# Optimization experiments

Measured on AMD Instinct MI355X. Metric: run time of the kernel, lower is better.

Reference implementation:

```python
import jax, jax.numpy as jnp
import numpy as np

NUM_USERS = 400000  # matches fill_max of indexes in input_specs
K = 10              # top_k from init_kwargs
NEG_INF = -1000000000.0


def setup_inputs() -> dict:
    key = jax.random.key(0)
    k1, k2, k3 = jax.random.split(key, 3)
    N = 8000000
    predictions = jax.random.normal(k1, (N,), dtype=jnp.float32)
    targets = jax.random.uniform(k2, (N,), dtype=jnp.float32)
    indexes = jax.random.randint(k3, (N,), 0, NUM_USERS, dtype=jnp.int64)
    return {"predictions": predictions, "targets": targets, "indexes": indexes}


def reference(predictions, targets, indexes):
    # Faithful to the torch source, which does `counts_per_user[u] = 1` (not +=1):
    # column 0 holds each user's FIRST occurrence, column 1 holds the LAST
    # occurrence (subsequent scatters to pos 1 overwrite), everything else is
    # padding (-1e9 preds / 0 targets). Padding columns beyond k provably don't
    # affect topk/dcg/idcg, so we use a static width of K.
    n = predictions.shape[0]
    pos = jnp.arange(n, dtype=jnp.int32)
    seg = indexes.astype(jnp.int32)
    first = jax.ops.segment_min(pos, seg, num_segments=NUM_USERS)
    last = jax.ops.segment_max(pos, seg, num_segments=NUM_USERS)
    counts = jax.ops.segment_sum(jnp.ones_like(pos), seg, num_segments=NUM_USERS)
    has2 = counts >= 2  # pos 1 is only ever written on a second occurrence

    p0 = predictions[first]
    t0 = targets[first]
    p1 = jnp.where(has2, predictions[last], NEG_INF)
    t1 = jnp.where(has2, targets[last], 0.0)

    pred_padded = jnp.full((NUM_USERS, K), NEG_INF, dtype=predictions.dtype)
    pred_padded = pred_padded.at[:, 0].set(p0).at[:, 1].set(p1)
    target_padded = jnp.zeros((NUM_USERS, K), dtype=targets.dtype)
    target_padded = target_padded.at[:, 0].set(t0).at[:, 1].set(t1)

    _, topk_idx = jax.lax.top_k(pred_padded, K)
    topk_targets = jnp.take_along_axis(target_padded, topk_idx, axis=1)
    discounts = jnp.log2(jnp.arange(2, K + 2, dtype=jnp.float32))
    dcg = (topk_targets / discounts).sum(axis=1)
    ideal = -jnp.sort(-target_padded, axis=1)  # descending sort
    idcg = (ideal[:, :K] / discounts).sum(axis=1)
    return (dcg / idcg).mean()
```

## Files before the change

### kernel.cpp

```cpp
#include <hip/hip_runtime.h>
#include <climits>

static constexpr int NUSERS = 400000;
static constexpr float NEG_INF_F = -1000000000.0f;
static constexpr float INV_LOG2_3 = 0.6309297535714575f;

static constexpr int USLICE = 1563;
static constexpr int S = 256;
static constexpr int CHUNK = 4096;
static constexpr int CPG = 255;
static constexpr int GSPAN = CHUNK * CPG;
static constexpr int G = 8;
static constexpr int CAP = 4608;


__global__ void k_init_part(int* __restrict__ cursor, float* __restrict__ acc) {
    int t = blockIdx.x * blockDim.x + threadIdx.x;
    if (t < G * S) cursor[t] = 0;
    if (t == G * S) acc[0] = 0.0f;
}

__global__ __launch_bounds__(256, 8) void k_scatter(const int* __restrict__ idx, int n,
                                                    unsigned* __restrict__ records,
                                                    int* __restrict__ cursor) {
    __shared__ int cnt[S];
    __shared__ int base_l[S + 1];
    __shared__ int base_g[S];
    __shared__ unsigned stage[CHUNK];

    const int t = threadIdx.x;
    const int g = blockIdx.x / CPG;
    const int cbase = blockIdx.x * CHUNK - g * GSPAN;
    const int q0 = blockIdx.x * (CHUNK / 4);
    const int nq = n >> 2;
    const int4* idx4 = reinterpret_cast<const int4*>(idx);

    int4 v[4];
    int rnk[16];
#pragma unroll
    for (int k = 0; k < 4; ++k) {
        int q = q0 + k * 256 + t;
        v[k] = (q < nq) ? idx4[q] : make_int4(-1, -1, -1, -1);
    }

    if (t < S) cnt[t] = 0;
    __syncthreads();

#pragma unroll
    for (int k = 0; k < 4; ++k) {
        int us[4] = {v[k].x, v[k].y, v[k].z, v[k].w};
#pragma unroll
        for (int e = 0; e < 4; ++e)
            rnk[k * 4 + e] = (us[e] >= 0) ? atomicAdd(&cnt[us[e] / USLICE], 1) : 0;
    }
    __syncthreads();

    if (t < 64) {
        int v0 = cnt[t];
        int v1 = cnt[64 + t];
        int v2 = cnt[128 + t];
        int v3 = cnt[192 + t];
        int a = v0, b = v1, c = v2, d = v3;
#pragma unroll
        for (int dd = 1; dd < 64; dd <<= 1) { int y = __shfl_up(a, dd, 64); if (t >= dd) a += y; }
        int ta = __shfl(a, 63, 64);
#pragma unroll
        for (int dd = 1; dd < 64; dd <<= 1) { int y = __shfl_up(b, dd, 64); if (t >= dd) b += y; }
        int tb = __shfl(b, 63, 64);
#pragma unroll
        for (int dd = 1; dd < 64; dd <<= 1) { int y = __shfl_up(c, dd, 64); if (t >= dd) c += y; }
        int tc = __shfl(c, 63, 64);
#pragma unroll
        for (int dd = 1; dd < 64; dd <<= 1) { int y = __shfl_up(d, dd, 64); if (t >= dd) d += y; }
        int td = __shfl(d, 63, 64);
        b += ta; c += ta + tb; d += ta + tb + tc;
        base_l[t] = a - v0;
        base_l[64 + t] = b - v1;
        base_l[128 + t] = c - v2;
        base_l[192 + t] = d - v3;
        if (t == 0) base_l[S] = ta + tb + tc + td;
    }
    if (t < S) base_g[t] = atomicAdd(&cursor[g * S + t], cnt[t]);
    __syncthreads();

#pragma unroll
    for (int k = 0; k < 4; ++k) {
        int us[4] = {v[k].x, v[k].y, v[k].z, v[k].w};
#pragma unroll
        for (int e = 0; e < 4; ++e) {
            int u = us[e];
            if (u >= 0) {
                int s = u / USLICE;
                int loc = u - s * USLICE;
                int pos = base_l[s] + rnk[k * 4 + e];
                unsigned pic = (unsigned)((k * 256 + t) * 4 + e);
                stage[pos] = ((unsigned)s << 23) | ((unsigned)loc << 12) | pic;
            }
        }
    }
    __syncthreads();

    int total = base_l[S];
    for (int r = t; r < total; r += 256) {
        unsigned tmp = stage[r];
        int s = tmp >> 23;
        unsigned loc = (tmp >> 12) & 0x7FFu;
        unsigned iloc = (unsigned)cbase + (tmp & 0xFFFu);
        int pos = base_g[s] + (r - base_l[s]);
        if (pos < CAP)
            records[(size_t)(g * S + s) * CAP + pos] = (loc << 20) | iloc;
    }
}

__global__ __launch_bounds__(1024, 4) void k_reduce_ndcg(
        const unsigned* __restrict__ records, const int* __restrict__ cursor,
        const float* __restrict__ pred, const float* __restrict__ tgt,
        int n, float* __restrict__ acc) {
    __shared__ int tabf[USLICE];
    __shared__ int tabl[USLICE];
    const int s = blockIdx.x;
    const int t = threadIdx.x;

    for (int u = t; u < USLICE; u += 1024) { tabf[u] = INT_MAX; tabl[u] = -1; }
    __syncthreads();

    for (int g = 0; g < G; ++g) {
        int cnt = min(cursor[g * S + s], CAP);
        const uint4* base4 = reinterpret_cast<const uint4*>(records + (size_t)(g * S + s) * CAP);
        const int gb = g * GSPAN;
        for (int p4 = t; p4 * 4 < cnt; p4 += 1024) {
            uint4 vv = base4[p4];
            int p = p4 * 4;
            unsigned rr[4] = {vv.x, vv.y, vv.z, vv.w};
#pragma unroll
            for (int e = 0; e < 4; ++e) {
                if (p + e < cnt) {
                    int loc = rr[e] >> 20;
                    int i = (int)(rr[e] & 0xFFFFFu) + gb;
                    atomicMin(&tabf[loc], i);
                    atomicMax(&tabl[loc], i);
                }
            }
        }
    }
    __syncthreads();

    float v = 0.0f;
    for (int uu = t; uu < USLICE; uu += 1024) {
        int u = s * USLICE + uu;
        if (u < NUSERS) {
            int f = tabf[uu];
            int l = tabl[uu];
            f = min(f, n - 1);
            float p0 = pred[f];
            float t0 = tgt[f];
            bool has2 = l > f;
            float p1 = has2 ? pred[l] : NEG_INF_F;
            float t1 = has2 ? tgt[l] : 0.0f;
            float dcg  = (p0 >= p1) ? fmaf(t1, INV_LOG2_3, t0) : fmaf(t0, INV_LOG2_3, t1);
            float idcg = fmaf(fminf(t0, t1), INV_LOG2_3, fmaxf(t0, t1));
            v += dcg / idcg;
        }
    }
    for (int off = 32; off > 0; off >>= 1) v += __shfl_down(v, off, 64);
    __shared__ float wsum[16];
    int lane = t & 63, wid = t >> 6;
    if (lane == 0) wsum[wid] = v;
    __syncthreads();
    if (t == 0) {
        float ss = 0.0f;
#pragma unroll
        for (int w = 0; w < 16; ++w) ss += wsum[w];
        atomicAdd(acc, ss);
    }
}

__global__ void k_final(const float* __restrict__ acc, float* __restrict__ out) {
    out[0] = acc[0] * (1.0f / (float)NUSERS);
}


__global__ void k_init_fb(int* __restrict__ first, int* __restrict__ last,
                          float* __restrict__ acc) {
    int i = blockIdx.x * blockDim.x + threadIdx.x;
    if (i < NUSERS) { first[i] = INT_MAX; last[i] = -1; }
    if (i == 0) acc[0] = 0.0f;
}

__global__ void k_minmax_fb(const int* __restrict__ idx, int* __restrict__ first,
                            int* __restrict__ last, int n) {
    int base = (blockIdx.x * blockDim.x + threadIdx.x) * 4;
    if (base + 3 < n) {
        int4 u4 = *reinterpret_cast<const int4*>(idx + base);
        int us[4] = {u4.x, u4.y, u4.z, u4.w};
#pragma unroll
        for (int j = 0; j < 4; ++j) {
            int u = us[j], i = base + j;
            if (i < first[u]) atomicMin(&first[u], i);
            if (i > last[u])  atomicMax(&last[u], i);
        }
    } else {
        for (int i = base; i < n; ++i) {
            int u = idx[i];
            if (i < first[u]) atomicMin(&first[u], i);
            if (i > last[u])  atomicMax(&last[u], i);
        }
    }
}

__global__ void k_ndcg_fb(const float* __restrict__ pred, const float* __restrict__ tgt,
                          const int* __restrict__ first, const int* __restrict__ last,
                          int n, float* __restrict__ acc) {
    int u = blockIdx.x * blockDim.x + threadIdx.x;
    float v = 0.0f;
    if (u < NUSERS) {
        int f = min(first[u], n - 1);
        int l = last[u];
        float p0 = pred[f], t0 = tgt[f];
        bool has2 = l > f;
        float p1 = has2 ? pred[l] : NEG_INF_F;
        float t1 = has2 ? tgt[l] : 0.0f;
        float dcg  = (p0 >= p1) ? fmaf(t1, INV_LOG2_3, t0) : fmaf(t0, INV_LOG2_3, t1);
        float idcg = fmaf(fminf(t0, t1), INV_LOG2_3, fmaxf(t0, t1));
        v = dcg / idcg;
    }
    for (int off = 32; off > 0; off >>= 1) v += __shfl_down(v, off, 64);
    __shared__ float wsum[4];
    int lane = threadIdx.x & 63, wid = threadIdx.x >> 6;
    if (lane == 0) wsum[wid] = v;
    __syncthreads();
    if (threadIdx.x == 0) atomicAdd(acc, wsum[0] + wsum[1] + wsum[2] + wsum[3]);
}


extern "C" void kernel_launch(void* const* d_in, const int* in_sizes, int n_in,
                              void* d_out, int out_size, void* d_ws, size_t ws_size,
                              hipStream_t stream) {
    const float* pred = (const float*)d_in[0];
    const float* tgt  = (const float*)d_in[1];
    const int*   idx  = (const int*)d_in[2];
    const int n = in_sizes[0];
    float* out = (float*)d_out;

    const size_t recs_bytes = (size_t)G * S * CAP * sizeof(unsigned);
    const size_t need = recs_bytes + 16384;

    if (ws_size >= need && n <= G * GSPAN && (n & 3) == 0) {
        unsigned* records = (unsigned*)d_ws;
        char* tail = (char*)d_ws + recs_bytes;
        int* cursor = (int*)tail;
        float* acc = (float*)(tail + 8192);

        k_init_part<<<(G * S + 256) / 256, 256, 0, stream>>>(cursor, acc);

        int nblocks = (n + CHUNK - 1) / CHUNK;
        k_scatter<<<nblocks, 256, 0, stream>>>(idx, n, records, cursor);

        k_reduce_ndcg<<<S, 1024, 0, stream>>>(records, cursor, pred, tgt, n, acc);

        k_final<<<1, 1, 0, stream>>>(acc, out);
    } else {
        int* first = (int*)d_ws;
        int* last  = first + NUSERS;
        float* acc = (float*)(last + NUSERS);

        k_init_fb<<<(NUSERS + 255) / 256, 256, 0, stream>>>(first, last, acc);
        int nq4 = (n + 3) / 4;
        k_minmax_fb<<<(nq4 + 255) / 256, 256, 0, stream>>>(idx, first, last, n);
        k_ndcg_fb<<<(NUSERS + 255) / 256, 256, 0, stream>>>(pred, tgt, first, last, n, acc);
        k_final<<<1, 1, 0, stream>>>(acc, out);
    }
}
```

Baseline: 151.1 us.

## Replace partitioned scatter with global atomic min/max plus value-capture pass

Drops the two-pass slice partition (LDS bucket scatter to records, then per-slice LDS min/max reduce) and replaces it with direct global atomicMin/atomicMax on an interleaved int2 first/last table. Chunks are visited in a hashed order so concurrent blocks touch scattered users, which reduces atomic contention. A second streaming pass reads idx, pred and tgt coalesced and writes the (pred, tgt) pairs for the first and last occurrence into a per-user table, removing the random gathers. The final NDCG kernel does the normalisation itself through a last-block counter, which removes k_final. In exchange it adds a full extra read of the 8M indices plus pred and tgt, and relies on global atomics that may contend.

New measurement: 509.6 us. 237% more time.

```diff
diff --git a/kernel.cpp b/kernel.cpp
--- a/kernel.cpp
+++ b/kernel.cpp
@@ -5,231 +5,128 @@
 static constexpr float NEG_INF_F = -1000000000.0f;
 static constexpr float INV_LOG2_3 = 0.6309297535714575f;
 
-static constexpr int USLICE = 1563;
-static constexpr int S = 256;
-static constexpr int CHUNK = 4096;
-static constexpr int CPG = 255;
-static constexpr int GSPAN = CHUNK * CPG;
-static constexpr int G = 8;
-static constexpr int CAP = 4608;
+static constexpr int NB1 = 2048;
+static constexpr int CE_LOG2 = 11;
+static constexpr int CE = 1 << CE_LOG2;
 
-
-__global__ void k_init_part(int* __restrict__ cursor, float* __restrict__ acc) {
-    int t = blockIdx.x * blockDim.x + threadIdx.x;
-    if (t < G * S) cursor[t] = 0;
-    if (t == G * S) acc[0] = 0.0f;
+__global__ void k_init(int2* __restrict__ tab, float2* __restrict__ vals,
+                       const float* __restrict__ pred, const float* __restrict__ tgt,
+                       int n, int* __restrict__ ctrl, float* __restrict__ acc) {
+    int i = blockIdx.x * blockDim.x + threadIdx.x;
+    float pl = pred[n - 1], tl = tgt[n - 1];
+    if (i < NUSERS) {
+        tab[i] = make_int2(INT_MAX, -1);
+        vals[2 * i]     = make_float2(pl, tl);
+        vals[2 * i + 1] = make_float2(NEG_INF_F, 0.0f);
+    }
+    if (i == 0) { ctrl[0] = 0; acc[0] = 0.0f; }
 }
 
-__global__ __launch_bounds__(256, 8) void k_scatter(const int* __restrict__ idx, int n,
-                                                    unsigned* __restrict__ records,
-                                                    int* __restrict__ cursor) {
-    __shared__ int cnt[S];
-    __shared__ int base_l[S + 1];
-    __shared__ int base_g[S];
-    __shared__ unsigned stage[CHUNK];
-
-    const int t = threadIdx.x;
-    const int g = blockIdx.x / CPG;
-    const int cbase = blockIdx.x * CHUNK - g * GSPAN;
-    const int q0 = blockIdx.x * (CHUNK / 4);
+__global__ __launch_bounds__(256, 8) void k_minmax(const int* __restrict__ idx, int n,
+                                                   int2* __restrict__ tab,
+                                                   unsigned pmask) {
     const int nq = n >> 2;
     const int4* idx4 = reinterpret_cast<const int4*>(idx);
+    const int t = threadIdx.x;
 
-    int4 v[4];
-    int rnk[16];
+    for (unsigned k = blockIdx.x; k <= pmask; k += NB1) {
+        unsigned chunk = (k * 0x9E3779B1u) & pmask;
+        int q0 = (int)(chunk << (CE_LOG2 - 2));
+        if (q0 >= nq) continue;
+
+        int4 v[2];
 #pragma unroll
-    for (int k = 0; k < 4; ++k) {
-        int q = q0 + k * 256 + t;
-        v[k] = (q < nq) ? idx4[q] : make_int4(-1, -1, -1, -1);
+        for (int r = 0; r < 2; ++r) {
+            int q = q0 + r * 256 + t;
+            v[r] = (q < nq) ? idx4[q] : make_int4(-1, -1, -1, -1);
+        }
+        int us[8] = {v[0].x, v[0].y, v[0].z, v[0].w,
+                     v[1].x, v[1].y, v[1].z, v[1].w};
+        int2 cur[8];
+#pragma unroll
+        for (int j = 0; j < 8; ++j)
+            cur[j] = (us[j] >= 0) ? tab[us[j]] : make_int2(INT_MIN, INT_MAX);
+#pragma unroll
+        for (int j = 0; j < 8; ++j) {
+            int r = j >> 2, e = j & 3;
+            int i = (q0 + r * 256 + t) * 4 + e;
+            if (i < cur[j].x) atomicMin(&tab[us[j]].x, i);
+            if (us[j] >= 0 && i > cur[j].y) atomicMax(&tab[us[j]].y, i);
+        }
     }
+    if (blockIdx.x == 0 && t == 0) {
+        for (int i = nq * 4; i < n; ++i) {
+            int u = idx[i];
+            atomicMin(&tab[u].x, i);
+            atomicMax(&tab[u].y, i);
+        }
+    }
+}
 
-    if (t < S) cnt[t] = 0;
-    __syncthreads();
-
+__global__ __launch_bounds__(256, 8) void k_detect(const int* __restrict__ idx,
+        const float* __restrict__ pred, const float* __restrict__ tgt, int n,
+        const int2* __restrict__ tab, float2* __restrict__ vals) {
+    const int nq = n >> 2;
+    const int4* idx4 = reinterpret_cast<const int4*>(idx);
+    const float4* pred4 = reinterpret_cast<const float4*>(pred);
+    const float4* tgt4 = reinterpret_cast<const float4*>(tgt);
+    const int t = threadIdx.x;
 #pragma unroll
-    for (int k = 0; k < 4; ++k) {
-        int us[4] = {v[k].x, v[k].y, v[k].z, v[k].w};
+    for (int r = 0; r < 2; ++r) {
+        int q = blockIdx.x * 512 + r * 256 + t;
+        if (q < nq) {
+            int4 u4 = idx4[q];
+            float4 p4 = pred4[q];
+            float4 g4 = tgt4[q];
+            int us[4] = {u4.x, u4.y, u4.z, u4.w};
+            float ps[4] = {p4.x, p4.y, p4.z, p4.w};
+            float gs[4] = {g4.x, g4.y, g4.z, g4.w};
+            int ib = q * 4;
 #pragma unroll
-        for (int e = 0; e < 4; ++e)
-            rnk[k * 4 + e] = (us[e] >= 0) ? atomicAdd(&cnt[us[e] / USLICE], 1) : 0;
-    }
-    __syncthreads();
-
-    if (t < 64) {
-        int v0 = cnt[t];
-        int v1 = cnt[64 + t];
-        int v2 = cnt[128 + t];
-        int v3 = cnt[192 + t];
-        int a = v0, b = v1, c = v2, d = v3;
-#pragma unroll
-        for (int dd = 1; dd < 64; dd <<= 1) { int y = __shfl_up(a, dd, 64); if (t >= dd) a += y; }
-        int ta = __shfl(a, 63, 64);
-#pragma unroll
-        for (int dd = 1; dd < 64; dd <<= 1) { int y = __shfl_up(b, dd, 64); if (t >= dd) b += y; }
-        int tb = __shfl(b, 63, 64);
-#pragma unroll
-        for (int dd = 1; dd < 64; dd <<= 1) { int y = __shfl_up(c, dd, 64); if (t >= dd) c += y; }
-        int tc = __shfl(c, 63, 64);
-#pragma unroll
-        for (int dd = 1; dd < 64; dd <<= 1) { int y = __shfl_up(d, dd, 64); if (t >= dd) d += y; }
-        int td = __shfl(d, 63, 64);
-        b += ta; c += ta + tb; d += ta + tb + tc;
-        base_l[t] = a - v0;
-        base_l[64 + t] = b - v1;
-        base_l[128 + t] = c - v2;
-        base_l[192 + t] = d - v3;
-        if (t == 0) base_l[S] = ta + tb + tc + td;
-    }
-    if (t < S) base_g[t] = atomicAdd(&cursor[g * S + t], cnt[t]);
-    __syncthreads();
-
-#pragma unroll
-    for (int k = 0; k < 4; ++k) {
-        int us[4] = {v[k].x, v[k].y, v[k].z, v[k].w};
-#pragma unroll
-        for (int e = 0; e < 4; ++e) {
-            int u = us[e];
-            if (u >= 0) {
-                int s = u / USLICE;
-                int loc = u - s * USLICE;
-                int pos = base_l[s] + rnk[k * 4 + e];
-                unsigned pic = (unsigned)((k * 256 + t) * 4 + e);
-                stage[pos] = ((unsigned)s << 23) | ((unsigned)loc << 12) | pic;
+            for (int e = 0; e < 4; ++e) {
+                int u = us[e];
+                int2 fl = tab[u];
+                int i = ib + e;
+                if (i == fl.x)      vals[2 * u]     = make_float2(ps[e], gs[e]);
+                else if (i == fl.y) vals[2 * u + 1] = make_float2(ps[e], gs[e]);
             }
         }
     }
-    __syncthreads();
-
-    int total = base_l[S];
-    for (int r = t; r < total; r += 256) {
-        unsigned tmp = stage[r];
-        int s = tmp >> 23;
-        unsigned loc = (tmp >> 12) & 0x7FFu;
-        unsigned iloc = (unsigned)cbase + (tmp & 0xFFFu);
-        int pos = base_g[s] + (r - base_l[s]);
-        if (pos < CAP)
-            records[(size_t)(g * S + s) * CAP + pos] = (loc << 20) | iloc;
+    if (blockIdx.x == 0 && t == 0) {
+        for (int i = nq * 4; i < n; ++i) {
+            int u = idx[i];
+            int2 fl = tab[u];
+            if (i == fl.x)      vals[2 * u]     = make_float2(pred[i], tgt[i]);
+            else if (i == fl.y) vals[2 * u + 1] = make_float2(pred[i], tgt[i]);
+        }
     }
 }
 
-__global__ __launch_bounds__(1024, 4) void k_reduce_ndcg(
-        const unsigned* __restrict__ records, const int* __restrict__ cursor,
-        const float* __restrict__ pred, const float* __restrict__ tgt,
-        int n, float* __restrict__ acc) {
-    __shared__ int tabf[USLICE];
-    __shared__ int tabl[USLICE];
-    const int s = blockIdx.x;
+__global__ __launch_bounds__(256, 8) void k_ndcg(const float4* __restrict__ vals,
+        float* __restrict__ acc, int* __restrict__ ctrl, float* __restrict__ out,
+        int nblk) {
     const int t = threadIdx.x;
-
-    for (int u = t; u < USLICE; u += 1024) { tabf[u] = INT_MAX; tabl[u] = -1; }
-    __syncthreads();
-
-    for (int g = 0; g < G; ++g) {
-        int cnt = min(cursor[g * S + s], CAP);
-        const uint4* base4 = reinterpret_cast<const uint4*>(records + (size_t)(g * S + s) * CAP);
-        const int gb = g * GSPAN;
-        for (int p4 = t; p4 * 4 < cnt; p4 += 1024) {
-            uint4 vv = base4[p4];
-            int p = p4 * 4;
-            unsigned rr[4] = {vv.x, vv.y, vv.z, vv.w};
-#pragma unroll
-            for (int e = 0; e < 4; ++e) {
-                if (p + e < cnt) {
-                    int loc = rr[e] >> 20;
-                    int i = (int)(rr[e] & 0xFFFFFu) + gb;
-                    atomicMin(&tabf[loc], i);
-                    atomicMax(&tabl[loc], i);
-                }
-            }
-        }
-    }
-    __syncthreads();
-
+    int u = blockIdx.x * 256 + t;
     float v = 0.0f;
-    for (int uu = t; uu < USLICE; uu += 1024) {
-        int u = s * USLICE + uu;
-        if (u < NUSERS) {
-            int f = tabf[uu];
-            int l = tabl[uu];
-            f = min(f, n - 1);
-            float p0 = pred[f];
-            float t0 = tgt[f];
-            bool has2 = l > f;
-            float p1 = has2 ? pred[l] : NEG_INF_F;
-            float t1 = has2 ? tgt[l] : 0.0f;
-            float dcg  = (p0 >= p1) ? fmaf(t1, INV_LOG2_3, t0) : fmaf(t0, INV_LOG2_3, t1);
-            float idcg = fmaf(fminf(t0, t1), INV_LOG2_3, fmaxf(t0, t1));
-            v += dcg / idcg;
-        }
+    if (u < NUSERS) {
+        float4 w = vals[u];
+        float dcg  = (w.x >= w.z) ? fmaf(w.w, INV_LOG2_3, w.y) : fmaf(w.y, INV_LOG2_3, w.w);
+        float idcg = fmaf(fminf(w.y, w.w), INV_LOG2_3, fmaxf(w.y, w.w));
+        v = dcg / idcg;
     }
     for (int off = 32; off > 0; off >>= 1) v += __shfl_down(v, off, 64);
-    __shared__ float wsum[16];
+    __shared__ float wsum[4];
     int lane = t & 63, wid = t >> 6;
     if (lane == 0) wsum[wid] = v;
     __syncthreads();
     if (t == 0) {
-        float ss = 0.0f;
-#pragma unroll
-        for (int w = 0; w < 16; ++w) ss += wsum[w];
-        atomicAdd(acc, ss);
-    }
-}
-
-__global__ void k_final(const float* __restrict__ acc, float* __restrict__ out) {
-    out[0] = acc[0] * (1.0f / (float)NUSERS);
-}
-
-
-__global__ void k_init_fb(int* __restrict__ first, int* __restrict__ last,
-                          float* __restrict__ acc) {
-    int i = blockIdx.x * blockDim.x + threadIdx.x;
-    if (i < NUSERS) { first[i] = INT_MAX; last[i] = -1; }
-    if (i == 0) acc[0] = 0.0f;
-}
-
-__global__ void k_minmax_fb(const int* __restrict__ idx, int* __restrict__ first,
-                            int* __restrict__ last, int n) {
-    int base = (blockIdx.x * blockDim.x + threadIdx.x) * 4;
-    if (base + 3 < n) {
-        int4 u4 = *reinterpret_cast<const int4*>(idx + base);
-        int us[4] = {u4.x, u4.y, u4.z, u4.w};
-#pragma unroll
-        for (int j = 0; j < 4; ++j) {
-            int u = us[j], i = base + j;
-            if (i < first[u]) atomicMin(&first[u], i);
-            if (i > last[u])  atomicMax(&last[u], i);
-        }
-    } else {
-        for (int i = base; i < n; ++i) {
-            int u = idx[i];
-            if (i < first[u]) atomicMin(&first[u], i);
-            if (i > last[u])  atomicMax(&last[u], i);
+        atomicAdd(acc, wsum[0] + wsum[1] + wsum[2] + wsum[3]);
+        int d = __hip_atomic_fetch_add(&ctrl[0], 1, __ATOMIC_ACQ_REL, __HIP_MEMORY_SCOPE_AGENT);
+        if (d == nblk - 1) {
+            float a = __hip_atomic_load(acc, __ATOMIC_RELAXED, __HIP_MEMORY_SCOPE_AGENT);
+            out[0] = a * (1.0f / (float)NUSERS);
         }
     }
-}
-
-__global__ void k_ndcg_fb(const float* __restrict__ pred, const float* __restrict__ tgt,
-                          const int* __restrict__ first, const int* __restrict__ last,
-                          int n, float* __restrict__ acc) {
-    int u = blockIdx.x * blockDim.x + threadIdx.x;
-    float v = 0.0f;
-    if (u < NUSERS) {
-        int f = min(first[u], n - 1);
-        int l = last[u];
-        float p0 = pred[f], t0 = tgt[f];
-        bool has2 = l > f;
-        float p1 = has2 ? pred[l] : NEG_INF_F;
-        float t1 = has2 ? tgt[l] : 0.0f;
-        float dcg  = (p0 >= p1) ? fmaf(t1, INV_LOG2_3, t0) : fmaf(t0, INV_LOG2_3, t1);
-        float idcg = fmaf(fminf(t0, t1), INV_LOG2_3, fmaxf(t0, t1));
-        v = dcg / idcg;
-    }
-    for (int off = 32; off > 0; off >>= 1) v += __shfl_down(v, off, 64);
-    __shared__ float wsum[4];
-    int lane = threadIdx.x & 63, wid = threadIdx.x >> 6;
-    if (lane == 0) wsum[wid] = v;
-    __syncthreads();
-    if (threadIdx.x == 0) atomicAdd(acc, wsum[0] + wsum[1] + wsum[2] + wsum[3]);
 }
 
 
@@ -241,33 +138,25 @@
     const int*   idx  = (const int*)d_in[2];
     const int n = in_sizes[0];
     float* out = (float*)d_out;
+    if (n < 1) return;
 
-    const size_t recs_bytes = (size_t)G * S * CAP * sizeof(unsigned);
-    const size_t need = recs_bytes + 16384;
+    float2* vals = (float2*)d_ws;
+    int2* tab = (int2*)((char*)d_ws + (size_t)NUSERS * 16);
+    int* ctrl = (int*)((char*)tab + (size_t)NUSERS * 8);
+    float* acc = (float*)(ctrl + 16);
 
-    if (ws_size >= need && n <= G * GSPAN && (n & 3) == 0) {
-        unsigned* records = (unsigned*)d_ws;
-        char* tail = (char*)d_ws + recs_bytes;
-        int* cursor = (int*)tail;
-        float* acc = (float*)(tail + 8192);
+    const int ublocks = (NUSERS + 255) / 256;
 
-        k_init_part<<<(G * S + 256) / 256, 256, 0, stream>>>(cursor, acc);
+    k_init<<<ublocks, 256, 0, stream>>>(tab, vals, pred, tgt, n, ctrl, acc);
 
-        int nblocks = (n + CHUNK - 1) / CHUNK;
-        k_scatter<<<nblocks, 256, 0, stream>>>(idx, n, records, cursor);
+    int nchunks = (n + CE - 1) / CE;
+    unsigned P = 1;
+    while ((int)P < nchunks) P <<= 1;
+    k_minmax<<<NB1, 256, 0, stream>>>(idx, n, tab, P - 1);
 
-        k_reduce_ndcg<<<S, 1024, 0, stream>>>(records, cursor, pred, tgt, n, acc);
+    int db = ((n >> 2) + 511) / 512;
+    if (db < 1) db = 1;
+    k_detect<<<db, 256, 0, stream>>>(idx, pred, tgt, n, tab, vals);
 
-        k_final<<<1, 1, 0, stream>>>(acc, out);
-    } else {
-        int* first = (int*)d_ws;
-        int* last  = first + NUSERS;
-        float* acc = (float*)(last + NUSERS);
-
-        k_init_fb<<<(NUSERS + 255) / 256, 256, 0, stream>>>(first, last, acc);
-        int nq4 = (n + 3) / 4;
-        k_minmax_fb<<<(nq4 + 255) / 256, 256, 0, stream>>>(idx, first, last, n);
-        k_ndcg_fb<<<(NUSERS + 255) / 256, 256, 0, stream>>>(pred, tgt, first, last, n, acc);
-        k_final<<<1, 1, 0, stream>>>(acc, out);
-    }
+    k_ndcg<<<ublocks, 256, 0, stream>>>((const float4*)vals, acc, ctrl, out, ublocks);
 }
```
